# Optimization experiments

Measured on AMD Instinct MI355X. Metric: run time of the kernel, lower is better.

The kernel has to match this reference:

```python
import jax, jax.numpy as jnp
import numpy as np

D = 1024
H = 16
T = D // H  # head dim; attention() scales by sqrt(Q.size(2)) == sqrt(T)
B = 4
S = 2048


def setup_inputs() -> dict:
    key = jax.random.key(0)
    ks = jax.random.split(key, 11)
    lim = 1.0 / np.sqrt(D)  # nn.Linear default init range
    inp = {
        "Q": jax.random.normal(ks[0], (B, S, D), jnp.float32),
        "K": jax.random.normal(ks[1], (B, S, D), jnp.float32),
        "V": jax.random.normal(ks[2], (B, S, D), jnp.float32),
        # per-head Q/K/V projections, stacked: weight [h, t, d], bias [h, t]
        "Wq": jax.random.uniform(ks[3], (H, T, D), jnp.float32, -lim, lim),
        "bq": jax.random.uniform(ks[4], (H, T), jnp.float32, -lim, lim),
        "Wk": jax.random.uniform(ks[5], (H, T, D), jnp.float32, -lim, lim),
        "bk": jax.random.uniform(ks[6], (H, T), jnp.float32, -lim, lim),
        "Wv": jax.random.uniform(ks[7], (H, T, D), jnp.float32, -lim, lim),
        "bv": jax.random.uniform(ks[8], (H, T), jnp.float32, -lim, lim),
        # output projection d -> d
        "Wo": jax.random.uniform(ks[9], (D, D), jnp.float32, -lim, lim),
        "bo": jax.random.uniform(ks[10], (D,), jnp.float32, -lim, lim),
    }
    return inp


def reference(Q, K, V, Wq, bq, Wk, bk, Wv, bv, Wo, bo):
    # Per-head projections, batched over heads: [b, h, s, t]
    q = jnp.einsum("bsd,htd->bhst", Q, Wq) + bq[None, :, None, :]
    k = jnp.einsum("bsd,htd->bhst", K, Wk) + bk[None, :, None, :]
    v = jnp.einsum("bsd,htd->bhst", V, Wv) + bv[None, :, None, :]
    # scaled dot-product attention; scale uses head dim T (Q.size(2) in source)
    scores = jnp.einsum("bhqt,bhkt->bhqk", q, k) / jnp.sqrt(jnp.asarray(T, q.dtype))
    probs = jax.nn.softmax(scores, axis=-1)
    ctx = jnp.einsum("bhqk,bhkt->bhqt", probs, v)
    # concat heads along feature dim (head i -> slice [i*t:(i+1)*t])
    z = ctx.transpose(0, 2, 1, 3).reshape(B, S, D)
    return jnp.einsum("bsd,ed->bse", z, Wo) + bo
```

## Files before the change

### kernel.cpp

```cpp
#include <hip/hip_runtime.h>

typedef unsigned short u16;
typedef unsigned int u32;
typedef __bf16 bf16x8 __attribute__((ext_vector_type(8)));
typedef __bf16 bf16x2 __attribute__((ext_vector_type(2)));
typedef float f32x4 __attribute__((ext_vector_type(4)));

#define BB 4
#define SS 2048
#define DD 1024
#define HH 16
#define TT 64

#define QSCALE 0.18033688011112042f

__device__ __forceinline__ u16 f32_to_bf16(float f) {
    unsigned int u = __float_as_uint(f);
    u += 0x7fffu + ((u >> 16) & 1u);
    return (u16)(u >> 16);
}

__device__ __forceinline__ u32 pack_bf16x2(float a, float b) {
    bf16x2 t;
    t[0] = (__bf16)a;
    t[1] = (__bf16)b;
    return __builtin_bit_cast(u32, t);
}

#define GLDS(g, l) __builtin_amdgcn_global_load_lds(                              \
    (const __attribute__((address_space(1))) void*)(g),                            \
    (__attribute__((address_space(3))) void*)(l), 16, 0, 0)

struct PackArgs {
    const float* s[4];
    u16* d[4];
};

__global__ __launch_bounds__(256) void pack_multi(PackArgs a) {
    const float* __restrict__ src = a.s[blockIdx.y];
    u16* __restrict__ dst = a.d[blockIdx.y];
    int i = (blockIdx.x * 256 + threadIdx.x) * 8;
    float4 x = *(const float4*)(src + i);
    float4 y = *(const float4*)(src + i + 4);
    ushort4 o0, o1;
    o0.x = f32_to_bf16(x.x); o0.y = f32_to_bf16(x.y);
    o0.z = f32_to_bf16(x.z); o0.w = f32_to_bf16(x.w);
    o1.x = f32_to_bf16(y.x); o1.y = f32_to_bf16(y.y);
    o1.z = f32_to_bf16(y.z); o1.w = f32_to_bf16(y.w);
    *(ushort4*)(dst + i)     = o0;
    *(ushort4*)(dst + i + 4) = o1;
}

#define GEMM_CORE(Aptr, Wptr)                                                      \
    __shared__ u16 lds_a[128 * 64];                                                \
    __shared__ u16 lds_b[128 * 64];                                                \
    const int tid = threadIdx.x;                                                   \
    const int w = tid >> 6, l = tid & 63;                                          \
    const int bm = blockIdx.y * 128;                                               \
    const int bn = blockIdx.x * 128;                                               \
    const int wm = (w >> 1) * 64;                                                  \
    const int wn = (w & 1) * 64;                                                   \
    const int srow = l >> 3;                                                       \
    const int scol = (l & 7) * 16;                                                 \
    f32x4 acc[4][4] = {};                                                          \
    const char* Abase = (const char*)(Aptr) + (size_t)bm * 2048;                   \
    const char* Bbase = (const char*)(Wptr) + (size_t)bn * 2048;                   \
    for (int kt = 0; kt < 1024; kt += 64) {                                        \
        _Pragma("unroll")                                                          \
        for (int j = 0; j < 4; ++j) {                                              \
            int chunk = w * 4 + j;                                                 \
            int r = chunk * 8 + srow;                                              \
            int csrc = scol ^ ((r & 7) << 4);                                      \
            GLDS(Abase + (size_t)r * 2048 + kt * 2 + csrc, &lds_a[chunk * 512]);   \
            GLDS(Bbase + (size_t)r * 2048 + kt * 2 + csrc, &lds_b[chunk * 512]);   \
        }                                                                          \
        __syncthreads();                                                           \
        _Pragma("unroll")                                                          \
        for (int ks = 0; ks < 2; ++ks) {                                           \
            bf16x8 af[4], bfr[4];                                                  \
            _Pragma("unroll")                                                      \
            for (int i = 0; i < 4; ++i) {                                          \
                int ra = wm + i * 16 + (l & 15);                                   \
                int ba = (ks * 64 + ((l >> 4) << 4)) ^ ((ra & 7) << 4);            \
                af[i] = *(const bf16x8*)((const char*)lds_a + ra * 128 + ba);      \
                int rb = wn + i * 16 + (l & 15);                                   \
                int bb2 = (ks * 64 + ((l >> 4) << 4)) ^ ((rb & 7) << 4);           \
                bfr[i] = *(const bf16x8*)((const char*)lds_b + rb * 128 + bb2);    \
            }                                                                      \
            _Pragma("unroll")                                                      \
            for (int mi = 0; mi < 4; ++mi)                                         \
                _Pragma("unroll")                                                  \
                for (int ni = 0; ni < 4; ++ni)                                     \
                    acc[mi][ni] = __builtin_amdgcn_mfma_f32_16x16x32_bf16(         \
                        af[mi], bfr[ni], acc[mi][ni], 0, 0, 0);                    \
        }                                                                          \
        __syncthreads();                                                           \
    }

struct QkvArgs {
    const u16* A[3];
    const u16* W[3];
    const float* bias[3];
    u16* out[3];
};

__global__ __launch_bounds__(256, 2) void gemm_qkv(QkvArgs args) {
    const int mode = blockIdx.z;
    const u16* A = args.A[mode];
    const u16* Wp = args.W[mode];
    const float* bias = args.bias[mode];
    u16* Cb = args.out[mode];

    GEMM_CORE(A, Wp)

    const int mq = (l >> 4) << 2;
    const float scale = (mode == 0) ? QSCALE : 1.0f;
#pragma unroll
    for (int mi = 0; mi < 4; ++mi) {
#pragma unroll
        for (int ni = 0; ni < 4; ++ni) {
            int m0 = bm + wm + mi * 16 + mq;
            int n  = bn + wn + ni * 16 + (l & 15);
            float bv = bias[n];
            f32x4 v = acc[mi][ni];
            if (mode == 2) {
                int bi = m0 >> 11, s0 = m0 & 2047;
                int hi = n >> 6, t = n & 63;
                size_t base = ((size_t)((bi * 16 + hi) * 64 + t)) * 2048 + s0;
                ushort4 pk;
                pk.x = f32_to_bf16(v[0] + bv);
                pk.y = f32_to_bf16(v[1] + bv);
                pk.z = f32_to_bf16(v[2] + bv);
                pk.w = f32_to_bf16(v[3] + bv);
                *(ushort4*)(&Cb[base]) = pk;
            } else {
#pragma unroll
                for (int r = 0; r < 4; ++r) {
                    int m = m0 + r;
                    size_t addr = ((size_t)(((m >> 11) * 16 + (n >> 6)) * 2048 + (m & 2047))) * 64
                                  + (n & 63);
                    Cb[addr] = f32_to_bf16((v[r] + bv) * scale);
                }
            }
        }
    }
}

__global__ __launch_bounds__(256, 2) void gemm_out(
    const u16* __restrict__ A, const u16* __restrict__ Wp,
    const float* __restrict__ bias, float* __restrict__ Cf)
{
    GEMM_CORE(A, Wp)

    const int mq = (l >> 4) << 2;
#pragma unroll
    for (int mi = 0; mi < 4; ++mi) {
#pragma unroll
        for (int ni = 0; ni < 4; ++ni) {
            int m0 = bm + wm + mi * 16 + mq;
            int n  = bn + wn + ni * 16 + (l & 15);
            float bv = bias[n];
            f32x4 v = acc[mi][ni];
#pragma unroll
            for (int r = 0; r < 4; ++r)
                Cf[(size_t)(m0 + r) * 1024 + n] = v[r] + bv;
        }
    }
}

union PbU {
    u32 d[4];
    bf16x8 v;
};

__global__ __launch_bounds__(512, 4) void attn_kernel(
    const u16* __restrict__ qh,
    const u16* __restrict__ kh,
    const u16* __restrict__ vt,
    u16* __restrict__ z)
{
    __shared__ u16 k_lds[2][64 * 64];
    __shared__ u16 v_lds[2][64 * 64];
    __shared__ u16 p_lds[8][16 * 64];
    const int tid = threadIdx.x;
    const int w = tid >> 6, l = tid & 63;
    const int lq = l & 15, lh = l >> 4;
    const int bh = blockIdx.x;
    const int qb = blockIdx.y * 128;
    const size_t hbase = (size_t)bh * (2048 * 64);

    const int qrow = qb + w * 16 + lq;
    bf16x8 qf[2];
#pragma unroll
    for (int ks = 0; ks < 2; ++ks)
        qf[ks] = *(const bf16x8*)(qh + hbase + (size_t)qrow * 64 + ks * 32 + (lh << 3));

    f32x4 ctxT[4] = {};
    float mrow = -1e30f;
    float lsum = 0.f;

    const int sr = l >> 3;
    const int csrc = (((l & 7) ^ sr) << 4);
    const char* kp = (const char*)(kh + hbase) + (size_t)(w * 8 + sr) * 128 + csrc;
    const char* vp = (const char*)(vt + hbase) + (size_t)(w * 8 + sr) * 4096 + csrc;
    u16* kd[2] = { &k_lds[0][w * 512], &k_lds[1][w * 512] };
    u16* vd[2] = { &v_lds[0][w * 512], &v_lds[1][w * 512] };

    char* pw = (char*)&p_lds[w][0] + lq * 128;
    const int swz = ((lq & 7) << 4) ^ (lq & 8);

    GLDS(kp, kd[0]);
    GLDS(vp, vd[0]);
    kp += 8192; vp += 128;
    __syncthreads();

#define BODY(CB, NB, PF)                                                           \
    {                                                                              \
        if (PF) {                                                                  \
            GLDS(kp, kd[NB]);                                                      \
            GLDS(vp, vd[NB]);                                                      \
            kp += 8192; vp += 128;                                                 \
        }                                                                          \
        f32x4 sfr[4] = {};                                                         \
        __builtin_amdgcn_s_setprio(1);                                             \
        _Pragma("unroll")                                                          \
        for (int nb = 0; nb < 4; ++nb) {                                           \
            _Pragma("unroll")                                                      \
            for (int ks = 0; ks < 2; ++ks) {                                       \
                int rk = nb * 16 + lq;                                             \
                int by = (ks * 64 + (lh << 4)) ^ ((lq & 7) << 4);                  \
                bf16x8 kf = *(const bf16x8*)((const char*)k_lds[CB] + rk * 128 + by); \
                sfr[nb] = __builtin_amdgcn_mfma_f32_16x16x32_bf16(kf, qf[ks], sfr[nb], 0, 0, 0); \
            }                                                                      \
        }                                                                          \
        __builtin_amdgcn_s_setprio(0);                                             \
                                              \
        float c0 = fmaxf(fmaxf(fmaxf(sfr[0][0], sfr[1][0]), sfr[2][0]), sfr[3][0]); \
        float c1 = fmaxf(fmaxf(fmaxf(sfr[0][1], sfr[1][1]), sfr[2][1]), sfr[3][1]); \
        float c2 = fmaxf(fmaxf(fmaxf(sfr[0][2], sfr[1][2]), sfr[2][2]), sfr[3][2]); \
        float c3 = fmaxf(fmaxf(fmaxf(sfr[0][3], sfr[1][3]), sfr[2][3]), sfr[3][3]); \
        float mx = fmaxf(fmaxf(c0, c1), fmaxf(c2, c3));                            \
        mx = fmaxf(mx, __shfl_xor(mx, 16));                                        \
        mx = fmaxf(mx, __shfl_xor(mx, 32));                                        \
        if (__any(mx - mrow > 11.5f)) {         \
            float mnew = fmaxf(mrow, mx);                                          \
            float alpha = __builtin_amdgcn_exp2f(mrow - mnew);                     \
            mrow = mnew;                                                           \
            lsum *= alpha;                                                         \
            _Pragma("unroll")                                                      \
            for (int nb = 0; nb < 4; ++nb) ctxT[nb] *= alpha;                      \
        }                                                                          \
        u32 pk0[4], pk1[4];                                                        \
        float psum = 0.f;                                                          \
        _Pragma("unroll")                                                          \
        for (int nb = 0; nb < 4; ++nb) {                                           \
            float p0 = __builtin_amdgcn_exp2f(sfr[nb][0] - mrow);                  \
            float p1 = __builtin_amdgcn_exp2f(sfr[nb][1] - mrow);                  \
            float p2 = __builtin_amdgcn_exp2f(sfr[nb][2] - mrow);                  \
            float p3 = __builtin_amdgcn_exp2f(sfr[nb][3] - mrow);                  \
            psum += (p0 + p1) + (p2 + p3);                                         \
            pk0[nb] = pack_bf16x2(p0, p1);                                         \
            pk1[nb] = pack_bf16x2(p2, p3);                                         \
        }                                                                          \
        lsum += psum;                                                              \
                              \
        _Pragma("unroll")                                                          \
        for (int nb = 0; nb < 4; ++nb)                                             \
            *(uint2*)(pw + (((nb << 5) + (lh << 3)) ^ swz)) = make_uint2(pk0[nb], pk1[nb]); \
        asm volatile("s_waitcnt lgkmcnt(0)" ::: "memory");                         \
        __builtin_amdgcn_sched_barrier(0);                                         \
             \
        bf16x8 pb[2];                                                              \
        {                                                                          \
            int base0 = ((lh >> 1) << 5) + ((lh & 1) << 4);                        \
            uint2 lo0 = *(const uint2*)(pw + ((base0) ^ swz));                     \
            uint2 hi0 = *(const uint2*)(pw + ((base0 + 8) ^ swz));                 \
            uint2 lo1 = *(const uint2*)(pw + ((base0 + 64) ^ swz));                \
            uint2 hi1 = *(const uint2*)(pw + ((base0 + 72) ^ swz));                \
            PbU u0, u1;                                                            \
            u0.d[0] = lo0.x; u0.d[1] = lo0.y; u0.d[2] = hi0.x; u0.d[3] = hi0.y;    \
            u1.d[0] = lo1.x; u1.d[1] = lo1.y; u1.d[2] = hi1.x; u1.d[3] = hi1.y;    \
            pb[0] = u0.v; pb[1] = u1.v;                                            \
        }                                                                          \
        __builtin_amdgcn_s_setprio(1);                                             \
        _Pragma("unroll")                                                          \
        for (int nb = 0; nb < 4; ++nb) {                                           \
            _Pragma("unroll")                                                      \
            for (int ks = 0; ks < 2; ++ks) {                                       \
                int rv = nb * 16 + lq;                                             \
                int by = (ks * 64 + (lh << 4)) ^ ((lq & 7) << 4);                  \
                bf16x8 vf = *(const bf16x8*)((const char*)v_lds[CB] + rv * 128 + by); \
                ctxT[nb] = __builtin_amdgcn_mfma_f32_16x16x32_bf16(vf, pb[ks], ctxT[nb], 0, 0, 0); \
            }                                                                      \
        }                                                                          \
        __builtin_amdgcn_s_setprio(0);                                             \
        __syncthreads();                                                           \
    }

    for (int tt = 0; tt < 32; tt += 2) {
        BODY(0, 1, true)
        BODY(1, 0, (tt < 30))
    }
#undef BODY

    float rsum = lsum;
    rsum += __shfl_xor(rsum, 16);
    rsum += __shfl_xor(rsum, 32);
    float rinv = 1.0f / rsum;

    const int b = bh >> 4, h = bh & 15;
    u16* zrow = z + ((size_t)(b * 2048 + qrow)) * 1024 + h * 64 + lh * 4;
#pragma unroll
    for (int nb = 0; nb < 4; ++nb) {
        ushort4 o;
        o.x = f32_to_bf16(ctxT[nb][0] * rinv);
        o.y = f32_to_bf16(ctxT[nb][1] * rinv);
        o.z = f32_to_bf16(ctxT[nb][2] * rinv);
        o.w = f32_to_bf16(ctxT[nb][3] * rinv);
        *(ushort4*)(zrow + nb * 16) = o;
    }
}

extern "C" void kernel_launch(void* const* d_in, const int* in_sizes, int n_in,
                              void* d_out, int out_size, void* d_ws, size_t ws_size,
                              hipStream_t stream) {
    const float* Q  = (const float*)d_in[0];
    const float* K  = (const float*)d_in[1];
    const float* V  = (const float*)d_in[2];
    const float* Wq = (const float*)d_in[3];
    const float* bq = (const float*)d_in[4];
    const float* Wk = (const float*)d_in[5];
    const float* bk = (const float*)d_in[6];
    const float* Wv = (const float*)d_in[7];
    const float* bv = (const float*)d_in[8];
    const float* Wo = (const float*)d_in[9];
    const float* bo = (const float*)d_in[10];

    const int ACT = BB * SS * DD;
    const int WEL = DD * DD;

    u16* ws  = (u16*)d_ws;
    u16* Qb  = ws;
    u16* Kb  = Qb + ACT;
    u16* Vb  = Kb + ACT;
    u16* Wqb = Vb + ACT;
    u16* Wkb = Wqb + WEL;
    u16* Wvb = Wkb + WEL;
    u16* Wob = Wvb + WEL;
    u16* qhb = Wob + WEL;
    u16* khb = qhb + ACT;
    u16* vtb = khb + ACT;
    u16* zb  = vtb + ACT;

    PackArgs pa;
    pa.s[0] = Q;  pa.s[1] = K;  pa.s[2] = V;  pa.s[3] = nullptr;
    pa.d[0] = Qb; pa.d[1] = Kb; pa.d[2] = Vb; pa.d[3] = nullptr;
    pack_multi<<<dim3(ACT / 2048, 3), 256, 0, stream>>>(pa);

    PackArgs pb;
    pb.s[0] = Wq;  pb.s[1] = Wk;  pb.s[2] = Wv;  pb.s[3] = Wo;
    pb.d[0] = Wqb; pb.d[1] = Wkb; pb.d[2] = Wvb; pb.d[3] = Wob;
    pack_multi<<<dim3(WEL / 2048, 4), 256, 0, stream>>>(pb);

    QkvArgs qa;
    qa.A[0] = Qb;  qa.A[1] = Kb;  qa.A[2] = Vb;
    qa.W[0] = Wqb; qa.W[1] = Wkb; qa.W[2] = Wvb;
    qa.bias[0] = bq; qa.bias[1] = bk; qa.bias[2] = bv;
    qa.out[0] = qhb; qa.out[1] = khb; qa.out[2] = vtb;
    gemm_qkv<<<dim3(8, 64, 3), 256, 0, stream>>>(qa);

    attn_kernel<<<dim3(64, 16), 512, 0, stream>>>(qhb, khb, vtb, zb);

    gemm_out<<<dim3(8, 64), 256, 0, stream>>>(zb, Wob, bo, (float*)d_out);
}
```

Baseline: 224.3 us.

## Switch attention to 32x32x16 MFMA with register P-transpose via permlane32 swap

Rewrites the attention inner loop to use 32x32x16 bf16 MFMAs, with each wave owning 32 query rows and the block shrinking to 4 waves of 256 threads. The P matrix goes from the S accumulator layout into B-operand layout in registers using permlane32_swap, which removes the per-wave LDS round trip and its lgkmcnt wait. The aim is fewer LDS accesses and fewer, larger MFMA instructions per tile. In exchange each wave holds more accumulator registers, and fewer waves per block may lower occupancy and latency hiding.

```diff
diff --git a/kernel.cpp b/kernel.cpp
--- a/kernel.cpp
+++ b/kernel.cpp
@@ -5,6 +5,8 @@
 typedef __bf16 bf16x8 __attribute__((ext_vector_type(8)));
 typedef __bf16 bf16x2 __attribute__((ext_vector_type(2)));
 typedef float f32x4 __attribute__((ext_vector_type(4)));
+typedef float f32x16 __attribute__((ext_vector_type(16)));
+typedef unsigned int u32x2v __attribute__((ext_vector_type(2)));
 
 #define BB 4
 #define SS 2048
@@ -25,6 +27,22 @@
     t[0] = (__bf16)a;
     t[1] = (__bf16)b;
     return __builtin_bit_cast(u32, t);
+}
+
+__device__ __forceinline__ void pswap(u32& x, u32& y) {
+#if __has_builtin(__builtin_amdgcn_permlane32_swap)
+    u32x2v r = __builtin_amdgcn_permlane32_swap(x, y, false, false);
+    x = r[0];
+    y = r[1];
+#else
+    u32 sx = __shfl_xor(y, 32);
+    u32 sy = __shfl_xor(x, 32);
+    bool lo = (threadIdx.x & 32) == 0;
+    u32 nx = lo ? x : sx;
+    u32 ny = lo ? sy : y;
+    x = nx;
+    y = ny;
+#endif
 }
 
 #define GLDS(g, l) __builtin_amdgcn_global_load_lds(                              \
@@ -173,7 +191,7 @@
     bf16x8 v;
 };
 
-__global__ __launch_bounds__(512, 4) void attn_kernel(
+__global__ __launch_bounds__(256, 4) void attn_kernel(
     const u16* __restrict__ qh,
     const u16* __restrict__ kh,
     const u16* __restrict__ vt,
@@ -181,143 +199,140 @@
 {
     __shared__ u16 k_lds[2][64 * 64];
     __shared__ u16 v_lds[2][64 * 64];
-    __shared__ u16 p_lds[8][16 * 64];
     const int tid = threadIdx.x;
     const int w = tid >> 6, l = tid & 63;
-    const int lq = l & 15, lh = l >> 4;
+    const int l31 = l & 31, h2 = l >> 5;
     const int bh = blockIdx.x;
     const int qb = blockIdx.y * 128;
     const size_t hbase = (size_t)bh * (2048 * 64);
 
-    const int qrow = qb + w * 16 + lq;
-    bf16x8 qf[2];
-#pragma unroll
-    for (int ks = 0; ks < 2; ++ks)
-        qf[ks] = *(const bf16x8*)(qh + hbase + (size_t)qrow * 64 + ks * 32 + (lh << 3));
-
-    f32x4 ctxT[4] = {};
+    const int qrow = qb + w * 32 + l31;
+    bf16x8 qf[4];
+    {
+        const char* qp = (const char*)(qh + hbase) + (size_t)qrow * 128 + (h2 << 4);
+#pragma unroll
+        for (int ks = 0; ks < 4; ++ks)
+            qf[ks] = *(const bf16x8*)(qp + ks * 32);
+    }
+
+    f32x16 ctx0 = {}, ctx1 = {};
     float mrow = -1e30f;
     float lsum = 0.f;
 
     const int sr = l >> 3;
     const int csrc = (((l & 7) ^ sr) << 4);
-    const char* kp = (const char*)(kh + hbase) + (size_t)(w * 8 + sr) * 128 + csrc;
-    const char* vp = (const char*)(vt + hbase) + (size_t)(w * 8 + sr) * 4096 + csrc;
-    u16* kd[2] = { &k_lds[0][w * 512], &k_lds[1][w * 512] };
-    u16* vd[2] = { &v_lds[0][w * 512], &v_lds[1][w * 512] };
-
-    char* pw = (char*)&p_lds[w][0] + lq * 128;
-    const int swz = ((lq & 7) << 4) ^ (lq & 8);
-
-    GLDS(kp, kd[0]);
-    GLDS(vp, vd[0]);
-    kp += 8192; vp += 128;
+    const char* kp = (const char*)(kh + hbase) + (size_t)(w * 16 + sr) * 128 + csrc;
+    const char* vp = (const char*)(vt + hbase) + (size_t)(w * 16 + sr) * 4096 + csrc;
+    u16* kdst[2] = { &k_lds[0][w * 1024], &k_lds[1][w * 1024] };
+    u16* vdst[2] = { &v_lds[0][w * 1024], &v_lds[1][w * 1024] };
+
+#define ASTAGE(NB)                                                                 \
+    do {                                                                           \
+        GLDS(kp, kdst[NB]);          GLDS(kp + 1024, kdst[NB] + 512);              \
+        GLDS(vp, vdst[NB]);          GLDS(vp + 32768, vdst[NB] + 512);             \
+        kp += 8192; vp += 128;                                                     \
+    } while (0)
+
+    ASTAGE(0);
     __syncthreads();
 
-#define BODY(CB, NB, PF)                                                           \
+    const int swzrow = (l31 & 7) << 4;
+    const int colb = h2 << 4;
+
+#define ABODY(CB, NB, PF)                                                          \
     {                                                                              \
-        if (PF) {                                                                  \
-            GLDS(kp, kd[NB]);                                                      \
-            GLDS(vp, vd[NB]);                                                      \
-            kp += 8192; vp += 128;                                                 \
-        }                                                                          \
-        f32x4 sfr[4] = {};                                                         \
+        if (PF) ASTAGE(NB);                                                        \
+        f32x16 sfr0 = {}, sfr1 = {};                                               \
         __builtin_amdgcn_s_setprio(1);                                             \
         _Pragma("unroll")                                                          \
-        for (int nb = 0; nb < 4; ++nb) {                                           \
-            _Pragma("unroll")                                                      \
-            for (int ks = 0; ks < 2; ++ks) {                                       \
-                int rk = nb * 16 + lq;                                             \
-                int by = (ks * 64 + (lh << 4)) ^ ((lq & 7) << 4);                  \
-                bf16x8 kf = *(const bf16x8*)((const char*)k_lds[CB] + rk * 128 + by); \
-                sfr[nb] = __builtin_amdgcn_mfma_f32_16x16x32_bf16(kf, qf[ks], sfr[nb], 0, 0, 0); \
-            }                                                                      \
+        for (int ks = 0; ks < 4; ++ks) {                                           \
+            int by = ((ks << 5) + colb) ^ swzrow;                                  \
+            const char* kb0 = (const char*)k_lds[CB] + l31 * 128 + by;             \
+            bf16x8 kf0 = *(const bf16x8*)(kb0);                                    \
+            bf16x8 kf1 = *(const bf16x8*)(kb0 + 4096);                             \
+            sfr0 = __builtin_amdgcn_mfma_f32_32x32x16_bf16(kf0, qf[ks], sfr0, 0, 0, 0); \
+            sfr1 = __builtin_amdgcn_mfma_f32_32x32x16_bf16(kf1, qf[ks], sfr1, 0, 0, 0); \
         }                                                                          \
         __builtin_amdgcn_s_setprio(0);                                             \
-                                              \
-        float c0 = fmaxf(fmaxf(fmaxf(sfr[0][0], sfr[1][0]), sfr[2][0]), sfr[3][0]); \
-        float c1 = fmaxf(fmaxf(fmaxf(sfr[0][1], sfr[1][1]), sfr[2][1]), sfr[3][1]); \
-        float c2 = fmaxf(fmaxf(fmaxf(sfr[0][2], sfr[1][2]), sfr[2][2]), sfr[3][2]); \
-        float c3 = fmaxf(fmaxf(fmaxf(sfr[0][3], sfr[1][3]), sfr[2][3]), sfr[3][3]); \
-        float mx = fmaxf(fmaxf(c0, c1), fmaxf(c2, c3));                            \
-        mx = fmaxf(mx, __shfl_xor(mx, 16));                                        \
+                             \
+        float mx = fmaxf(sfr0[0], sfr1[0]);                                        \
+        _Pragma("unroll")                                                          \
+        for (int i = 1; i < 16; ++i) mx = fmaxf(mx, fmaxf(sfr0[i], sfr1[i]));      \
         mx = fmaxf(mx, __shfl_xor(mx, 32));                                        \
         if (__any(mx - mrow > 11.5f)) {         \
             float mnew = fmaxf(mrow, mx);                                          \
             float alpha = __builtin_amdgcn_exp2f(mrow - mnew);                     \
             mrow = mnew;                                                           \
             lsum *= alpha;                                                         \
-            _Pragma("unroll")                                                      \
-            for (int nb = 0; nb < 4; ++nb) ctxT[nb] *= alpha;                      \
-        }                                                                          \
-        u32 pk0[4], pk1[4];                                                        \
+            ctx0 *= alpha; ctx1 *= alpha;                                          \
+        }                                                                          \
+                 \
+        uint2 Qd0[4], Qd1[4];                                                      \
         float psum = 0.f;                                                          \
         _Pragma("unroll")                                                          \
-        for (int nb = 0; nb < 4; ++nb) {                                           \
-            float p0 = __builtin_amdgcn_exp2f(sfr[nb][0] - mrow);                  \
-            float p1 = __builtin_amdgcn_exp2f(sfr[nb][1] - mrow);                  \
-            float p2 = __builtin_amdgcn_exp2f(sfr[nb][2] - mrow);                  \
-            float p3 = __builtin_amdgcn_exp2f(sfr[nb][3] - mrow);                  \
-            psum += (p0 + p1) + (p2 + p3);                                         \
-            pk0[nb] = pack_bf16x2(p0, p1);                                         \
-            pk1[nb] = pack_bf16x2(p2, p3);                                         \
+        for (int m = 0; m < 4; ++m) {                                              \
+            float a0 = __builtin_amdgcn_exp2f(sfr0[4 * m + 0] - mrow);             \
+            float a1 = __builtin_amdgcn_exp2f(sfr0[4 * m + 1] - mrow);             \
+            float a2 = __builtin_amdgcn_exp2f(sfr0[4 * m + 2] - mrow);             \
+            float a3 = __builtin_amdgcn_exp2f(sfr0[4 * m + 3] - mrow);             \
+            float b0 = __builtin_amdgcn_exp2f(sfr1[4 * m + 0] - mrow);             \
+            float b1 = __builtin_amdgcn_exp2f(sfr1[4 * m + 1] - mrow);             \
+            float b2 = __builtin_amdgcn_exp2f(sfr1[4 * m + 2] - mrow);             \
+            float b3 = __builtin_amdgcn_exp2f(sfr1[4 * m + 3] - mrow);             \
+            psum += ((a0 + a1) + (a2 + a3)) + ((b0 + b1) + (b2 + b3));             \
+            Qd0[m] = make_uint2(pack_bf16x2(a0, a1), pack_bf16x2(a2, a3));         \
+            Qd1[m] = make_uint2(pack_bf16x2(b0, b1), pack_bf16x2(b2, b3));         \
         }                                                                          \
         lsum += psum;                                                              \
-                              \
-        _Pragma("unroll")                                                          \
-        for (int nb = 0; nb < 4; ++nb)                                             \
-            *(uint2*)(pw + (((nb << 5) + (lh << 3)) ^ swz)) = make_uint2(pk0[nb], pk1[nb]); \
-        asm volatile("s_waitcnt lgkmcnt(0)" ::: "memory");                         \
-        __builtin_amdgcn_sched_barrier(0);                                         \
-             \
-        bf16x8 pb[2];                                                              \
-        {                                                                          \
-            int base0 = ((lh >> 1) << 5) + ((lh & 1) << 4);                        \
-            uint2 lo0 = *(const uint2*)(pw + ((base0) ^ swz));                     \
-            uint2 hi0 = *(const uint2*)(pw + ((base0 + 8) ^ swz));                 \
-            uint2 lo1 = *(const uint2*)(pw + ((base0 + 64) ^ swz));                \
-            uint2 hi1 = *(const uint2*)(pw + ((base0 + 72) ^ swz));                \
-            PbU u0, u1;                                                            \
-            u0.d[0] = lo0.x; u0.d[1] = lo0.y; u0.d[2] = hi0.x; u0.d[3] = hi0.y;    \
-            u1.d[0] = lo1.x; u1.d[1] = lo1.y; u1.d[2] = hi1.x; u1.d[3] = hi1.y;    \
-            pb[0] = u0.v; pb[1] = u1.v;                                            \
-        }                                                                          \
+                         \
         __builtin_amdgcn_s_setprio(1);                                             \
         _Pragma("unroll")                                                          \
-        for (int nb = 0; nb < 4; ++nb) {                                           \
-            _Pragma("unroll")                                                      \
-            for (int ks = 0; ks < 2; ++ks) {                                       \
-                int rv = nb * 16 + lq;                                             \
-                int by = (ks * 64 + (lh << 4)) ^ ((lq & 7) << 4);                  \
-                bf16x8 vf = *(const bf16x8*)((const char*)v_lds[CB] + rv * 128 + by); \
-                ctxT[nb] = __builtin_amdgcn_mfma_f32_16x16x32_bf16(vf, pb[ks], ctxT[nb], 0, 0, 0); \
-            }                                                                      \
+        for (int ks = 0; ks < 4; ++ks) {                                           \
+            u32 x0, x1, y0, y1;                                                    \
+            if (ks == 0) { x0 = Qd0[0].x; x1 = Qd0[0].y; y0 = Qd0[1].x; y1 = Qd0[1].y; } \
+            else if (ks == 1) { x0 = Qd0[2].x; x1 = Qd0[2].y; y0 = Qd0[3].x; y1 = Qd0[3].y; } \
+            else if (ks == 2) { x0 = Qd1[0].x; x1 = Qd1[0].y; y0 = Qd1[1].x; y1 = Qd1[1].y; } \
+            else { x0 = Qd1[2].x; x1 = Qd1[2].y; y0 = Qd1[3].x; y1 = Qd1[3].y; }   \
+            pswap(x0, y0);                                                         \
+            pswap(x1, y1);                                                         \
+            PbU pu;                                                                \
+            pu.d[0] = x0; pu.d[1] = x1; pu.d[2] = y0; pu.d[3] = y1;                \
+            int by = ((ks << 5) + colb) ^ swzrow;                                  \
+            const char* vb0 = (const char*)v_lds[CB] + l31 * 128 + by;             \
+            bf16x8 vf0 = *(const bf16x8*)(vb0);                                    \
+            bf16x8 vf1 = *(const bf16x8*)(vb0 + 4096);                             \
+            ctx0 = __builtin_amdgcn_mfma_f32_32x32x16_bf16(vf0, pu.v, ctx0, 0, 0, 0); \
+            ctx1 = __builtin_amdgcn_mfma_f32_32x32x16_bf16(vf1, pu.v, ctx1, 0, 0, 0); \
         }                                                                          \
         __builtin_amdgcn_s_setprio(0);                                             \
         __syncthreads();                                                           \
     }
 
     for (int tt = 0; tt < 32; tt += 2) {
-        BODY(0, 1, true)
-        BODY(1, 0, (tt < 30))
-    }
-#undef BODY
-
-    float rsum = lsum;
-    rsum += __shfl_xor(rsum, 16);
-    rsum += __shfl_xor(rsum, 32);
+        ABODY(0, 1, true)
+        ABODY(1, 0, (tt < 30))
+    }
+#undef ABODY
+#undef ASTAGE
+
+    float rsum = lsum + __shfl_xor(lsum, 32);
     float rinv = 1.0f / rsum;
 
-    const int b = bh >> 4, h = bh & 15;
-    u16* zrow = z + ((size_t)(b * 2048 + qrow)) * 1024 + h * 64 + lh * 4;
-#pragma unroll
-    for (int nb = 0; nb < 4; ++nb) {
-        ushort4 o;
-        o.x = f32_to_bf16(ctxT[nb][0] * rinv);
-        o.y = f32_to_bf16(ctxT[nb][1] * rinv);
-        o.z = f32_to_bf16(ctxT[nb][2] * rinv);
-        o.w = f32_to_bf16(ctxT[nb][3] * rinv);
-        *(ushort4*)(zrow + nb * 16) = o;
+    const int b = bh >> 4, hd = bh & 15;
+    u16* zrow = z + ((size_t)(b * 2048 + qrow)) * 1024 + hd * 64 + (h2 << 2);
+#pragma unroll
+    for (int m = 0; m < 4; ++m) {
+        ushort4 o0, o1;
+        o0.x = f32_to_bf16(ctx0[4 * m + 0] * rinv);
+        o0.y = f32_to_bf16(ctx0[4 * m + 1] * rinv);
+        o0.z = f32_to_bf16(ctx0[4 * m + 2] * rinv);
+        o0.w = f32_to_bf16(ctx0[4 * m + 3] * rinv);
+        o1.x = f32_to_bf16(ctx1[4 * m + 0] * rinv);
+        o1.y = f32_to_bf16(ctx1[4 * m + 1] * rinv);
+        o1.z = f32_to_bf16(ctx1[4 * m + 2] * rinv);
+        o1.w = f32_to_bf16(ctx1[4 * m + 3] * rinv);
+        *(ushort4*)(zrow + 8 * m)      = o0;
+        *(ushort4*)(zrow + 8 * m + 32) = o1;
     }
 }
 
@@ -369,7 +384,7 @@
     qa.out[0] = qhb; qa.out[1] = khb; qa.out[2] = vtb;
     gemm_qkv<<<dim3(8, 64, 3), 256, 0, stream>>>(qa);
 
-    attn_kernel<<<dim3(64, 16), 512, 0, stream>>>(qhb, khb, vtb, zb);
+    attn_kernel<<<dim3(64, 16), 256, 0, stream>>>(qhb, khb, vtb, zb);
 
     gemm_out<<<dim3(8, 64), 256, 0, stream>>>(zb, Wob, bo, (float*)d_out);
 }
```

Result: faster. 217.1 us (-3.2%).
